# Kernel optimization log

Hardware: AMD Instinct MI355X
Metric: run time of the kernel (lower is better)

The kernel has to match this reference:

```python
import jax, jax.numpy as jnp
import numpy as np

B, T, DIM = 4, 2048, 1024
H, DH = 16, 64  # num_heads, dim_head; weight_dim = H*DH = 1024
SCALE = DIM ** (-0.5)  # note: original scales by dim**-0.5, not dim_head**-0.5


def setup_inputs() -> dict:
    key = jax.random.key(0)
    k1, k2, k3 = jax.random.split(key, 3)
    x = jax.random.normal(k1, (B, T, DIM), dtype=jnp.float32)
    w_qkv = jax.random.normal(k2, (3 * H * DH, DIM), dtype=jnp.float32) * (DIM ** -0.5)
    w_out = jax.random.normal(k3, (DIM, H * DH), dtype=jnp.float32) * ((H * DH) ** -0.5)
    b_out = jnp.zeros((DIM,), dtype=jnp.float32)
    return {"x": x, "w_qkv": w_qkv, "w_out": w_out, "b_out": b_out}


def reference(x, w_qkv, w_out, b_out):
    # qkv: [b, t, 3*H*DH] (torch Linear: x @ W^T)
    qkv = jnp.einsum('btc,oc->bto', x, w_qkv)
    # rearrange 'b t (d k h) -> k b h t d' with k=3, h=H: d is the OUTERMOST
    # factor of the flattened axis, then k, then h (h fastest-varying).
    qkv = qkv.reshape(B, T, DH, 3, H)          # [b, t, d, k, h]
    qkv = jnp.transpose(qkv, (3, 0, 4, 1, 2))   # [k, b, h, t, d]
    q, k, v = qkv[0], qkv[1], qkv[2]
    # scores: [b, h, t, t]
    attn = jnp.einsum('bhid,bhjd->bhij', q, k) * SCALE
    attn = jax.nn.softmax(attn, axis=-1)
    out = jnp.einsum('bhij,bhjd->bhid', attn, v)           # [b, h, t, d]
    out = jnp.transpose(out, (0, 2, 1, 3)).reshape(B, T, H * DH)  # 'b h t d -> b t (h d)'
    return jnp.einsum('btc,oc->bto', out, w_out) + b_out
```

## Files before the change

### kernel.cpp

```cpp
#include <hip/hip_runtime.h>
#include <hip/hip_bf16.h>


typedef __attribute__((ext_vector_type(8))) short short8;
typedef __attribute__((ext_vector_type(4))) float floatx4;
typedef __attribute__((ext_vector_type(16))) float floatx16;

static __device__ __forceinline__ floatx4 mfma16(short8 a, short8 b, floatx4 c) {
    return __builtin_amdgcn_mfma_f32_16x16x32_bf16(a, b, c, 0, 0, 0);
}
static __device__ __forceinline__ floatx16 mfma32(short8 a, short8 b, floatx16 c) {
    return __builtin_amdgcn_mfma_f32_32x32x16_bf16(a, b, c, 0, 0, 0);
}

static __device__ __forceinline__ unsigned short f2bf_bits(float f) {
    __hip_bfloat16 h = __float2bfloat16(f);
    return *reinterpret_cast<unsigned short*>(&h);
}

static __device__ __forceinline__ float fast_exp2(float x) {
#if __has_builtin(__builtin_amdgcn_exp2f)
    return __builtin_amdgcn_exp2f(x);
#else
    return exp2f(x);
#endif
}

static __device__ __forceinline__ unsigned cvt_pk_bf16(float lo, float hi) {
    unsigned r;
    asm("v_cvt_pk_bf16_f32 %0, %1, %2" : "=v"(r) : "v"(lo), "v"(hi));
    return r;
}

static __device__ __forceinline__ void plane32_swap(unsigned& x, unsigned& y) {
#if __has_builtin(__builtin_amdgcn_permlane32_swap)
    typedef unsigned int uintx2 __attribute__((ext_vector_type(2)));
    uintx2 r = __builtin_amdgcn_permlane32_swap(x, y, false, false);
    x = r[0];
    y = r[1];
#else
    asm volatile("v_permlane32_swap_b32 %0, %1" : "+v"(x), "+v"(y));
#endif
}

#define GLD16(gptr, ldsptr)                                                  \
    __builtin_amdgcn_global_load_lds(                                        \
        (const __attribute__((address_space(1))) void*)(gptr),               \
        (__attribute__((address_space(3))) void*)(ldsptr), 16, 0, 0)

__global__ __launch_bounds__(256) void k_cvt(
    const float* __restrict__ src, unsigned short* __restrict__ dst, int n4)
{
    typedef __attribute__((ext_vector_type(4))) unsigned short ushort4v;
    for (int i = blockIdx.x * blockDim.x + threadIdx.x; i < n4;
         i += gridDim.x * blockDim.x) {
        const float4 v = ((const float4*)src)[i];
        ushort4v o;
        o.x = f2bf_bits(v.x);
        o.y = f2bf_bits(v.y);
        o.z = f2bf_bits(v.z);
        o.w = f2bf_bits(v.w);
        ((ushort4v*)dst)[i] = o;
    }
}

__global__ __launch_bounds__(256) void k_qkv(
    const unsigned short* __restrict__ x,
    const unsigned short* __restrict__ wq,
    unsigned short* __restrict__ qb,
    unsigned short* __restrict__ kb,
    unsigned short* __restrict__ vb)
{
    __shared__ unsigned short SM[16384];

    const int tid  = threadIdx.x;
    const int wave = tid >> 6, lane = tid & 63;
    const int quad = lane >> 4, l16 = lane & 15;
    const int wm = wave >> 1, wn = wave & 1;

    const int fid  = blockIdx.y * 24 + blockIdx.x;
    const int nfid = (fid & 7) * 192 + (fid >> 3);
    const int bx = nfid % 24;
    const int m0 = (nfid / 24) * 128;
    const int kk = bx >> 3;
    const int cb = bx & 7;

    const int srow = lane >> 2;
    const int sc8  = (lane & 3) * 8;
    const int row0 = wave * 32 + srow;
    const int row1 = row0 + 16;
    int bn0, bn1;
    if (kk < 2) {
        bn0 = (row0 & 63) * 48 + kk * 16 + cb * 2 + (row0 >> 6);
        bn1 = (row1 & 63) * 48 + kk * 16 + cb * 2 + (row1 >> 6);
    } else {
        bn0 = (cb * 8 + (row0 >> 4)) * 48 + 32 + (row0 & 15);
        bn1 = (cb * 8 + (row1 >> 4)) * 48 + 32 + (row1 & 15);
    }

    floatx4 acc[4][4];
#pragma unroll
    for (int i = 0; i < 4; i++)
#pragma unroll
        for (int j = 0; j < 4; j++) acc[i][j] = (floatx4){0.f, 0.f, 0.f, 0.f};

#define QKV_STAGE(BUF, K0)                                                        \
    do {                                                                          \
        GLD16(&x[(m0 + row0) * 1024 + (K0) + sc8],                                \
              &SM[(BUF) * 8192 + (wave * 32) * 32]);                              \
        GLD16(&x[(m0 + row1) * 1024 + (K0) + sc8],                                \
              &SM[(BUF) * 8192 + (wave * 32 + 16) * 32]);                         \
        GLD16(&wq[bn0 * 1024 + (K0) + sc8],                                       \
              &SM[(BUF) * 8192 + 4096 + (wave * 32) * 32]);                       \
        GLD16(&wq[bn1 * 1024 + (K0) + sc8],                                       \
              &SM[(BUF) * 8192 + 4096 + (wave * 32 + 16) * 32]);                  \
    } while (0)

    QKV_STAGE(0, 0);
    int buf = 0;
    for (int k0 = 0; k0 < 1024; k0 += 32) {
        __syncthreads();
        if (k0 + 32 < 1024) QKV_STAGE(buf ^ 1, k0 + 32);

        const unsigned short* Ab = &SM[buf * 8192];
        const unsigned short* Bb = &SM[buf * 8192 + 4096];
        short8 af[4], bfv[4];
#pragma unroll
        for (int mi = 0; mi < 4; mi++)
            af[mi] = *(const short8*)&Ab[(wm * 64 + mi * 16 + l16) * 32 + quad * 8];
#pragma unroll
        for (int ni = 0; ni < 4; ni++)
            bfv[ni] = *(const short8*)&Bb[(wn * 64 + ni * 16 + l16) * 32 + quad * 8];
#pragma unroll
        for (int mi = 0; mi < 4; mi++)
#pragma unroll
            for (int ni = 0; ni < 4; ni++)
                acc[mi][ni] = mfma16(af[mi], bfv[ni], acc[mi][ni]);
        buf ^= 1;
    }
    __syncthreads();

    if (kk == 2) {
#pragma unroll
        for (int ni = 0; ni < 4; ni++) {
            const int d = cb * 8 + wn * 4 + ni;
#pragma unroll
            for (int mi = 0; mi < 4; mi++) {
                const int m  = m0 + wm * 64 + mi * 16 + quad * 4;
                const int b  = m >> 11;
                const int tt = m & 2047;
                ushort4 pk;
                pk.x = f2bf_bits(acc[mi][ni][0]);
                pk.y = f2bf_bits(acc[mi][ni][1]);
                pk.z = f2bf_bits(acc[mi][ni][2]);
                pk.w = f2bf_bits(acc[mi][ni][3]);
                *(ushort4*)&vb[((b * 16 + l16) * 64 + d) * 2048 + tt] = pk;
            }
        }
    } else {
        const float scale = (kk == 0) ? 0.045084220027780106f : 1.0f;
        unsigned short* dst = (kk == 0) ? qb : kb;
        const int b = m0 >> 11, tt0 = m0 & 2047;
#pragma unroll
        for (int s = 0; s < 2; s++) {
            if (wn == s) {
#pragma unroll
                for (int ni = 0; ni < 4; ni++) {
                    const int d = ni * 16 + l16;
#pragma unroll
                    for (int mi = 0; mi < 4; mi++) {
                        const int tl = wm * 64 + mi * 16 + quad * 4;
#pragma unroll
                        for (int r = 0; r < 4; r++)
                            SM[(tl + r) * 72 + d] = f2bf_bits(acc[mi][ni][r] * scale);
                    }
                }
            }
            __syncthreads();
#pragma unroll
            for (int u = 0; u < 4; u++) {
                const int w  = tid + u * 256;
                const int tl = w >> 3;
                const int ch = (w & 7) * 8;
                *(uint4*)&dst[((b * 16 + cb * 2 + s) * 2048 + tt0 + tl) * 64 + ch] =
                    *(const uint4*)&SM[tl * 72 + ch];
            }
            __syncthreads();
        }
    }
#undef QKV_STAGE
}

__global__ __launch_bounds__(256, 2) void k_attn(
    const unsigned short* __restrict__ qt,
    const unsigned short* __restrict__ kt,
    const unsigned short* __restrict__ vg,
    __hip_bfloat16* __restrict__ og)
{
    __shared__ unsigned short Ks[64 * 72];
    __shared__ unsigned short Vt[64 * 72];

    const int tid  = threadIdx.x;
    const int wave = tid >> 6, lane = tid & 63;
    const int l31  = lane & 31, hi = lane >> 5;
    const int blk = blockIdx.x;
    const int bh  = (blk & 7) | ((blk >> 6) << 3);
    const int q0  = ((blk >> 3) & 7) * 256;
    const int qr  = q0 + wave * 64;

    short8 qf[2][4];
#pragma unroll
    for (int qb2 = 0; qb2 < 2; qb2++)
#pragma unroll
        for (int ks = 0; ks < 4; ks++)
            qf[qb2][ks] = *(const short8*)
                &qt[(bh * 2048 + qr + qb2 * 32 + l31) * 64 + ks * 16 + hi * 8];

    float lsum[2] = {0.f, 0.f};
    floatx16 o[2][2];
#pragma unroll
    for (int qb2 = 0; qb2 < 2; qb2++)
#pragma unroll
        for (int db = 0; db < 2; db++)
#pragma unroll
            for (int r = 0; r < 16; r++) o[qb2][db][r] = 0.f;

    const int sr = tid >> 2, sc = (tid & 3) * 16;

    uint4 rka = *(const uint4*)&kt[(bh * 2048 + sr) * 64 + sc];
    uint4 rkb = *(const uint4*)&kt[(bh * 2048 + sr) * 64 + sc + 8];
    uint4 rva = *(const uint4*)&vg[(bh * 64 + sr) * 2048 + sc];
    uint4 rvb = *(const uint4*)&vg[(bh * 64 + sr) * 2048 + sc + 8];

    for (int j0 = 0; j0 < 2048; j0 += 64) {
        *(uint4*)&Ks[sr * 72 + sc]     = rka;
        *(uint4*)&Ks[sr * 72 + sc + 8] = rkb;
        *(uint4*)&Vt[sr * 72 + sc]     = rva;
        *(uint4*)&Vt[sr * 72 + sc + 8] = rvb;
        __syncthreads();
        if (j0 + 64 < 2048) {
            rka = *(const uint4*)&kt[(bh * 2048 + j0 + 64 + sr) * 64 + sc];
            rkb = *(const uint4*)&kt[(bh * 2048 + j0 + 64 + sr) * 64 + sc + 8];
            rva = *(const uint4*)&vg[(bh * 64 + sr) * 2048 + j0 + 64 + sc];
            rvb = *(const uint4*)&vg[(bh * 64 + sr) * 2048 + j0 + 64 + sc + 8];
        }

#pragma unroll
        for (int kb2 = 0; kb2 < 2; kb2++) {
            short8 kf[4];
#pragma unroll
            for (int ks = 0; ks < 4; ks++)
                kf[ks] = *(const short8*)
                    &Ks[(kb2 * 32 + l31) * 72 + ks * 16 + hi * 8];

            floatx16 st[2];
#pragma unroll
            for (int qb2 = 0; qb2 < 2; qb2++)
#pragma unroll
                for (int r = 0; r < 16; r++) st[qb2][r] = 0.f;
            __builtin_amdgcn_s_setprio(1);
#pragma unroll
            for (int ks = 0; ks < 4; ks++)
#pragma unroll
                for (int qb2 = 0; qb2 < 2; qb2++)
                    st[qb2] = mfma32(kf[ks], qf[qb2][ks], st[qb2]);
            __builtin_amdgcn_s_setprio(0);

            short8 paf[2][2];
#pragma unroll
            for (int qb2 = 0; qb2 < 2; qb2++) {
                float p[16];
#pragma unroll
                for (int r = 0; r < 16; r++) p[r] = fast_exp2(st[qb2][r]);
                lsum[qb2] += ((p[0] + p[1]) + (p[2] + p[3])) +
                             ((p[4] + p[5]) + (p[6] + p[7])) +
                             ((p[8] + p[9]) + (p[10] + p[11])) +
                             ((p[12] + p[13]) + (p[14] + p[15]));
#pragma unroll
                for (int hf = 0; hf < 2; hf++) {
                    const int r0 = hf * 8;
                    unsigned c01 = cvt_pk_bf16(p[r0 + 0], p[r0 + 1]);
                    unsigned c23 = cvt_pk_bf16(p[r0 + 2], p[r0 + 3]);
                    unsigned c45 = cvt_pk_bf16(p[r0 + 4], p[r0 + 5]);
                    unsigned c67 = cvt_pk_bf16(p[r0 + 6], p[r0 + 7]);
                    plane32_swap(c01, c45);
                    plane32_swap(c23, c67);
                    uint4 t4 = {c01, c23, c45, c67};
                    paf[qb2][hf] = *reinterpret_cast<short8*>(&t4);
                }
            }

            short8 vf[2][2];
#pragma unroll
            for (int db = 0; db < 2; db++)
#pragma unroll
                for (int hf = 0; hf < 2; hf++)
                    vf[db][hf] = *(const short8*)
                        &Vt[(db * 32 + l31) * 72 + kb2 * 32 + hf * 16 + hi * 8];
            __builtin_amdgcn_s_setprio(1);
#pragma unroll
            for (int qb2 = 0; qb2 < 2; qb2++)
#pragma unroll
                for (int db = 0; db < 2; db++)
#pragma unroll
                    for (int hf = 0; hf < 2; hf++)
                        o[qb2][db] = mfma32(paf[qb2][hf], vf[db][hf], o[qb2][db]);
            __builtin_amdgcn_s_setprio(0);
        }
        __syncthreads();
    }

    lsum[0] += __shfl_xor(lsum[0], 32);
    lsum[1] += __shfl_xor(lsum[1], 32);

    const int b = bh >> 4, h = bh & 15;
#pragma unroll
    for (int qb2 = 0; qb2 < 2; qb2++) {
#pragma unroll
        for (int r = 0; r < 16; r++) {
            const int qrl = (r & 3) + 8 * (r >> 2) + 4 * hi;
            const float inv = 1.0f / __shfl(lsum[qb2], qrl);
            const int t = qr + qb2 * 32 + qrl;
#pragma unroll
            for (int db = 0; db < 2; db++)
                og[(b * 2048 + t) * 1024 + h * 64 + db * 32 + l31] =
                    __float2bfloat16(o[qb2][db][r] * inv);
        }
    }
}

__global__ __launch_bounds__(256) void k_out(
    const unsigned short* __restrict__ a,
    const unsigned short* __restrict__ wq,
    const float* __restrict__ bias,
    float* __restrict__ out)
{
    __shared__ unsigned short SM[16384];

    const int tid  = threadIdx.x;
    const int wave = tid >> 6, lane = tid & 63;
    const int quad = lane >> 4, l16 = lane & 15;
    const int wm = wave >> 1, wn = wave & 1;

    const int fid  = blockIdx.y * 8 + blockIdx.x;
    const int nfid = (fid & 7) * 64 + (fid >> 3);
    const int n0 = (nfid & 7) * 128;
    const int m0 = (nfid >> 3) * 128;

    const int srow = lane >> 2;
    const int sc8  = (lane & 3) * 8;
    const int row0 = wave * 32 + srow;
    const int row1 = row0 + 16;

    floatx4 acc[4][4];
#pragma unroll
    for (int i = 0; i < 4; i++)
#pragma unroll
        for (int j = 0; j < 4; j++) acc[i][j] = (floatx4){0.f, 0.f, 0.f, 0.f};

#define OUT_STAGE(BUF, K0)                                                        \
    do {                                                                          \
        GLD16(&a[(m0 + row0) * 1024 + (K0) + sc8],                                \
              &SM[(BUF) * 8192 + (wave * 32) * 32]);                              \
        GLD16(&a[(m0 + row1) * 1024 + (K0) + sc8],                                \
              &SM[(BUF) * 8192 + (wave * 32 + 16) * 32]);                         \
        GLD16(&wq[(n0 + row0) * 1024 + (K0) + sc8],                               \
              &SM[(BUF) * 8192 + 4096 + (wave * 32) * 32]);                       \
        GLD16(&wq[(n0 + row1) * 1024 + (K0) + sc8],                               \
              &SM[(BUF) * 8192 + 4096 + (wave * 32 + 16) * 32]);                  \
    } while (0)

    OUT_STAGE(0, 0);
    int buf = 0;
    for (int k0 = 0; k0 < 1024; k0 += 32) {
        __syncthreads();
        if (k0 + 32 < 1024) OUT_STAGE(buf ^ 1, k0 + 32);

        const unsigned short* Ab = &SM[buf * 8192];
        const unsigned short* Bb = &SM[buf * 8192 + 4096];
        short8 af[4], bfv[4];
#pragma unroll
        for (int mi = 0; mi < 4; mi++)
            af[mi] = *(const short8*)&Ab[(wm * 64 + mi * 16 + l16) * 32 + quad * 8];
#pragma unroll
        for (int ni = 0; ni < 4; ni++)
            bfv[ni] = *(const short8*)&Bb[(wn * 64 + ni * 16 + l16) * 32 + quad * 8];
#pragma unroll
        for (int mi = 0; mi < 4; mi++)
#pragma unroll
            for (int ni = 0; ni < 4; ni++)
                acc[mi][ni] = mfma16(af[mi], bfv[ni], acc[mi][ni]);
        buf ^= 1;
    }
#undef OUT_STAGE

#pragma unroll
    for (int ni = 0; ni < 4; ni++) {
        const int col = n0 + wn * 64 + ni * 16 + l16;
        const float bv = bias[col];
#pragma unroll
        for (int mi = 0; mi < 4; mi++) {
            const int mbase = m0 + wm * 64 + mi * 16 + quad * 4;
#pragma unroll
            for (int r = 0; r < 4; r++)
                out[(mbase + r) * 1024 + col] = acc[mi][ni][r] + bv;
        }
    }
}

extern "C" void kernel_launch(void* const* d_in, const int* in_sizes, int n_in,
                              void* d_out, int out_size, void* d_ws, size_t ws_size,
                              hipStream_t stream) {
    const float* x    = (const float*)d_in[0];
    const float* wqkv = (const float*)d_in[1];
    const float* wout = (const float*)d_in[2];
    const float* bout = (const float*)d_in[3];
    float* out = (float*)d_out;

    unsigned short* ws = (unsigned short*)d_ws;
    unsigned short* xb    = ws;
    unsigned short* wqkvb = xb + 8388608;
    unsigned short* woutb = wqkvb + 3145728;
    unsigned short* qb    = woutb + 1048576;
    unsigned short* kb    = qb + 8388608;
    unsigned short* vb    = kb + 8388608;
    unsigned short* ob    = vb + 8388608;

    k_cvt<<<2048, 256, 0, stream>>>(x,    xb,    8388608 / 4);
    k_cvt<<<1024, 256, 0, stream>>>(wqkv, wqkvb, 3145728 / 4);
    k_cvt<<<512,  256, 0, stream>>>(wout, woutb, 1048576 / 4);

    k_qkv<<<dim3(24, 64), 256, 0, stream>>>(xb, wqkvb, qb, kb, vb);
    k_attn<<<512, 256, 0, stream>>>(qb, kb, vb, (__hip_bfloat16*)ob);
    k_out<<<dim3(8, 64), 256, 0, stream>>>(ob, woutb, bout, out);
}
```

Measured before the change: 254.2 us.

## Halve attention query tile per wave to double grid and occupancy

Each wave in the attention kernel now handles 32 query rows instead of 64, so each block covers 128 queries. The grid doubles to 1024 blocks and launch bounds ask for 4 blocks per CU. This cuts register pressure and is meant to hide latency through more resident waves. In exchange, every K/V tile is loaded and staged in LDS twice as often per query, and each wave does fewer MFMAs per LDS read.

After: 281.8 us. 1.11x slower.

```diff
diff --git a/kernel.cpp b/kernel.cpp
--- a/kernel.cpp
+++ b/kernel.cpp
@@ -191,7 +191,7 @@
 #undef QKV_STAGE
 }
 
-__global__ __launch_bounds__(256, 2) void k_attn(
+__global__ __launch_bounds__(256, 4) void k_attn(
     const unsigned short* __restrict__ qt,
     const unsigned short* __restrict__ kt,
     const unsigned short* __restrict__ vg,
@@ -204,26 +204,22 @@
     const int wave = tid >> 6, lane = tid & 63;
     const int l31  = lane & 31, hi = lane >> 5;
     const int blk = blockIdx.x;
-    const int bh  = (blk & 7) | ((blk >> 6) << 3);
-    const int q0  = ((blk >> 3) & 7) * 256;
-    const int qr  = q0 + wave * 64;
-
-    short8 qf[2][4];
-#pragma unroll
-    for (int qb2 = 0; qb2 < 2; qb2++)
-#pragma unroll
-        for (int ks = 0; ks < 4; ks++)
-            qf[qb2][ks] = *(const short8*)
-                &qt[(bh * 2048 + qr + qb2 * 32 + l31) * 64 + ks * 16 + hi * 8];
-
-    float lsum[2] = {0.f, 0.f};
-    floatx16 o[2][2];
-#pragma unroll
-    for (int qb2 = 0; qb2 < 2; qb2++)
-#pragma unroll
-        for (int db = 0; db < 2; db++)
-#pragma unroll
-            for (int r = 0; r < 16; r++) o[qb2][db][r] = 0.f;
+    const int bh  = (blk & 7) | ((blk >> 7) << 3);
+    const int q0  = ((blk >> 3) & 15) * 128;
+    const int qr  = q0 + wave * 32;
+
+    short8 qf[4];
+#pragma unroll
+    for (int ks = 0; ks < 4; ks++)
+        qf[ks] = *(const short8*)
+            &qt[(bh * 2048 + qr + l31) * 64 + ks * 16 + hi * 8];
+
+    float lsum = 0.f;
+    floatx16 o[2];
+#pragma unroll
+    for (int db = 0; db < 2; db++)
+#pragma unroll
+        for (int r = 0; r < 16; r++) o[db][r] = 0.f;
 
     const int sr = tid >> 2, sc = (tid & 3) * 16;
 
@@ -253,41 +249,34 @@
                 kf[ks] = *(const short8*)
                     &Ks[(kb2 * 32 + l31) * 72 + ks * 16 + hi * 8];
 
-            floatx16 st[2];
-#pragma unroll
-            for (int qb2 = 0; qb2 < 2; qb2++)
-#pragma unroll
-                for (int r = 0; r < 16; r++) st[qb2][r] = 0.f;
+            floatx16 st;
+#pragma unroll
+            for (int r = 0; r < 16; r++) st[r] = 0.f;
             __builtin_amdgcn_s_setprio(1);
 #pragma unroll
             for (int ks = 0; ks < 4; ks++)
-#pragma unroll
-                for (int qb2 = 0; qb2 < 2; qb2++)
-                    st[qb2] = mfma32(kf[ks], qf[qb2][ks], st[qb2]);
+                st = mfma32(kf[ks], qf[ks], st);
             __builtin_amdgcn_s_setprio(0);
 
-            short8 paf[2][2];
-#pragma unroll
-            for (int qb2 = 0; qb2 < 2; qb2++) {
-                float p[16];
-#pragma unroll
-                for (int r = 0; r < 16; r++) p[r] = fast_exp2(st[qb2][r]);
-                lsum[qb2] += ((p[0] + p[1]) + (p[2] + p[3])) +
-                             ((p[4] + p[5]) + (p[6] + p[7])) +
-                             ((p[8] + p[9]) + (p[10] + p[11])) +
-                             ((p[12] + p[13]) + (p[14] + p[15]));
-#pragma unroll
-                for (int hf = 0; hf < 2; hf++) {
-                    const int r0 = hf * 8;
-                    unsigned c01 = cvt_pk_bf16(p[r0 + 0], p[r0 + 1]);
-                    unsigned c23 = cvt_pk_bf16(p[r0 + 2], p[r0 + 3]);
-                    unsigned c45 = cvt_pk_bf16(p[r0 + 4], p[r0 + 5]);
-                    unsigned c67 = cvt_pk_bf16(p[r0 + 6], p[r0 + 7]);
-                    plane32_swap(c01, c45);
-                    plane32_swap(c23, c67);
-                    uint4 t4 = {c01, c23, c45, c67};
-                    paf[qb2][hf] = *reinterpret_cast<short8*>(&t4);
-                }
+            float p[16];
+#pragma unroll
+            for (int r = 0; r < 16; r++) p[r] = fast_exp2(st[r]);
+            lsum += (((p[0] + p[1]) + (p[2] + p[3])) +
+                     ((p[4] + p[5]) + (p[6] + p[7]))) +
+                    (((p[8] + p[9]) + (p[10] + p[11])) +
+                     ((p[12] + p[13]) + (p[14] + p[15])));
+            short8 paf[2];
+#pragma unroll
+            for (int hf = 0; hf < 2; hf++) {
+                const int r0 = hf * 8;
+                unsigned c01 = cvt_pk_bf16(p[r0 + 0], p[r0 + 1]);
+                unsigned c23 = cvt_pk_bf16(p[r0 + 2], p[r0 + 3]);
+                unsigned c45 = cvt_pk_bf16(p[r0 + 4], p[r0 + 5]);
+                unsigned c67 = cvt_pk_bf16(p[r0 + 6], p[r0 + 7]);
+                plane32_swap(c01, c45);
+                plane32_swap(c23, c67);
+                uint4 t4 = {c01, c23, c45, c67};
+                paf[hf] = *reinterpret_cast<short8*>(&t4);
             }
 
             short8 vf[2][2];
@@ -299,33 +288,27 @@
                         &Vt[(db * 32 + l31) * 72 + kb2 * 32 + hf * 16 + hi * 8];
             __builtin_amdgcn_s_setprio(1);
 #pragma unroll
-            for (int qb2 = 0; qb2 < 2; qb2++)
-#pragma unroll
-                for (int db = 0; db < 2; db++)
-#pragma unroll
-                    for (int hf = 0; hf < 2; hf++)
-                        o[qb2][db] = mfma32(paf[qb2][hf], vf[db][hf], o[qb2][db]);
+            for (int db = 0; db < 2; db++)
+#pragma unroll
+                for (int hf = 0; hf < 2; hf++)
+                    o[db] = mfma32(paf[hf], vf[db][hf], o[db]);
             __builtin_amdgcn_s_setprio(0);
         }
         __syncthreads();
     }
 
-    lsum[0] += __shfl_xor(lsum[0], 32);
-    lsum[1] += __shfl_xor(lsum[1], 32);
+    lsum += __shfl_xor(lsum, 32);
 
     const int b = bh >> 4, h = bh & 15;
 #pragma unroll
-    for (int qb2 = 0; qb2 < 2; qb2++) {
-#pragma unroll
-        for (int r = 0; r < 16; r++) {
-            const int qrl = (r & 3) + 8 * (r >> 2) + 4 * hi;
-            const float inv = 1.0f / __shfl(lsum[qb2], qrl);
-            const int t = qr + qb2 * 32 + qrl;
-#pragma unroll
-            for (int db = 0; db < 2; db++)
-                og[(b * 2048 + t) * 1024 + h * 64 + db * 32 + l31] =
-                    __float2bfloat16(o[qb2][db][r] * inv);
-        }
+    for (int r = 0; r < 16; r++) {
+        const int qrl = (r & 3) + 8 * (r >> 2) + 4 * hi;
+        const float inv = 1.0f / __shfl(lsum, qrl);
+        const int t = qr + qrl;
+#pragma unroll
+        for (int db = 0; db < 2; db++)
+            og[(b * 2048 + t) * 1024 + h * 64 + db * 32 + l31] =
+                __float2bfloat16(o[db][r] * inv);
     }
 }
 
@@ -431,6 +414,6 @@
     k_cvt<<<512,  256, 0, stream>>>(wout, woutb, 1048576 / 4);
 
     k_qkv<<<dim3(24, 64), 256, 0, stream>>>(xb, wqkvb, qb, kb, vb);
-    k_attn<<<512, 256, 0, stream>>>(qb, kb, vb, (__hip_bfloat16*)ob);
+    k_attn<<<1024, 256, 0, stream>>>(qb, kb, vb, (__hip_bfloat16*)ob);
     k_out<<<dim3(8, 64), 256, 0, stream>>>(ob, woutb, bout, out);
 }
```

## Load K/V fragments directly from global memory, dropping LDS staging and barriers

Applied to the files above, without the earlier changes.

The attention kernel stops staging K and V tiles through shared memory with register prefetch and block barriers. Each wave now reads its MFMA K and V fragments straight from global memory, relying on L2/L1 caching, and processes 32 keys per iteration with an unroll of 2. This removes LDS traffic and __syncthreads, but each of the four waves now fetches the same K/V data separately. It also loses the explicit prefetch overlap, so global load latency may be exposed.

Result: slower. 312.1 us (+22.8%).

```diff
diff --git a/kernel.cpp b/kernel.cpp
--- a/kernel.cpp
+++ b/kernel.cpp
@@ -197,9 +197,6 @@
     const unsigned short* __restrict__ vg,
     __hip_bfloat16* __restrict__ og)
 {
-    __shared__ unsigned short Ks[64 * 72];
-    __shared__ unsigned short Vt[64 * 72];
-
     const int tid  = threadIdx.x;
     const int wave = tid >> 6, lane = tid & 63;
     const int l31  = lane & 31, hi = lane >> 5;
@@ -225,89 +222,70 @@
 #pragma unroll
             for (int r = 0; r < 16; r++) o[qb2][db][r] = 0.f;
 
-    const int sr = tid >> 2, sc = (tid & 3) * 16;
-
-    uint4 rka = *(const uint4*)&kt[(bh * 2048 + sr) * 64 + sc];
-    uint4 rkb = *(const uint4*)&kt[(bh * 2048 + sr) * 64 + sc + 8];
-    uint4 rva = *(const uint4*)&vg[(bh * 64 + sr) * 2048 + sc];
-    uint4 rvb = *(const uint4*)&vg[(bh * 64 + sr) * 2048 + sc + 8];
-
-    for (int j0 = 0; j0 < 2048; j0 += 64) {
-        *(uint4*)&Ks[sr * 72 + sc]     = rka;
-        *(uint4*)&Ks[sr * 72 + sc + 8] = rkb;
-        *(uint4*)&Vt[sr * 72 + sc]     = rva;
-        *(uint4*)&Vt[sr * 72 + sc + 8] = rvb;
-        __syncthreads();
-        if (j0 + 64 < 2048) {
-            rka = *(const uint4*)&kt[(bh * 2048 + j0 + 64 + sr) * 64 + sc];
-            rkb = *(const uint4*)&kt[(bh * 2048 + j0 + 64 + sr) * 64 + sc + 8];
-            rva = *(const uint4*)&vg[(bh * 64 + sr) * 2048 + j0 + 64 + sc];
-            rvb = *(const uint4*)&vg[(bh * 64 + sr) * 2048 + j0 + 64 + sc + 8];
+    const unsigned short* kbase = &kt[bh * 2048 * 64];
+    const unsigned short* vbase = &vg[bh * 64 * 2048];
+
+#pragma unroll 2
+    for (int j = 0; j < 2048; j += 32) {
+        short8 kf[4];
+#pragma unroll
+        for (int ks = 0; ks < 4; ks++)
+            kf[ks] = *(const short8*)&kbase[(j + l31) * 64 + ks * 16 + hi * 8];
+
+        floatx16 st[2];
+#pragma unroll
+        for (int qb2 = 0; qb2 < 2; qb2++)
+#pragma unroll
+            for (int r = 0; r < 16; r++) st[qb2][r] = 0.f;
+        __builtin_amdgcn_s_setprio(1);
+#pragma unroll
+        for (int ks = 0; ks < 4; ks++)
+#pragma unroll
+            for (int qb2 = 0; qb2 < 2; qb2++)
+                st[qb2] = mfma32(kf[ks], qf[qb2][ks], st[qb2]);
+        __builtin_amdgcn_s_setprio(0);
+
+        short8 vf[2][2];
+#pragma unroll
+        for (int db = 0; db < 2; db++)
+#pragma unroll
+            for (int hf = 0; hf < 2; hf++)
+                vf[db][hf] = *(const short8*)
+                    &vbase[(db * 32 + l31) * 2048 + j + hf * 16 + hi * 8];
+
+        short8 paf[2][2];
+#pragma unroll
+        for (int qb2 = 0; qb2 < 2; qb2++) {
+            float p[16];
+#pragma unroll
+            for (int r = 0; r < 16; r++) p[r] = fast_exp2(st[qb2][r]);
+            lsum[qb2] += (((p[0] + p[1]) + (p[2] + p[3])) +
+                          ((p[4] + p[5]) + (p[6] + p[7]))) +
+                         (((p[8] + p[9]) + (p[10] + p[11])) +
+                          ((p[12] + p[13]) + (p[14] + p[15])));
+#pragma unroll
+            for (int hf = 0; hf < 2; hf++) {
+                const int r0 = hf * 8;
+                unsigned c01 = cvt_pk_bf16(p[r0 + 0], p[r0 + 1]);
+                unsigned c23 = cvt_pk_bf16(p[r0 + 2], p[r0 + 3]);
+                unsigned c45 = cvt_pk_bf16(p[r0 + 4], p[r0 + 5]);
+                unsigned c67 = cvt_pk_bf16(p[r0 + 6], p[r0 + 7]);
+                plane32_swap(c01, c45);
+                plane32_swap(c23, c67);
+                uint4 t4 = {c01, c23, c45, c67};
+                paf[qb2][hf] = *reinterpret_cast<short8*>(&t4);
+            }
         }
 
-#pragma unroll
-        for (int kb2 = 0; kb2 < 2; kb2++) {
-            short8 kf[4];
-#pragma unroll
-            for (int ks = 0; ks < 4; ks++)
-                kf[ks] = *(const short8*)
-                    &Ks[(kb2 * 32 + l31) * 72 + ks * 16 + hi * 8];
-
-            floatx16 st[2];
-#pragma unroll
-            for (int qb2 = 0; qb2 < 2; qb2++)
-#pragma unroll
-                for (int r = 0; r < 16; r++) st[qb2][r] = 0.f;
-            __builtin_amdgcn_s_setprio(1);
-#pragma unroll
-            for (int ks = 0; ks < 4; ks++)
-#pragma unroll
-                for (int qb2 = 0; qb2 < 2; qb2++)
-                    st[qb2] = mfma32(kf[ks], qf[qb2][ks], st[qb2]);
-            __builtin_amdgcn_s_setprio(0);
-
-            short8 paf[2][2];
-#pragma unroll
-            for (int qb2 = 0; qb2 < 2; qb2++) {
-                float p[16];
-#pragma unroll
-                for (int r = 0; r < 16; r++) p[r] = fast_exp2(st[qb2][r]);
-                lsum[qb2] += ((p[0] + p[1]) + (p[2] + p[3])) +
-                             ((p[4] + p[5]) + (p[6] + p[7])) +
-                             ((p[8] + p[9]) + (p[10] + p[11])) +
-                             ((p[12] + p[13]) + (p[14] + p[15]));
-#pragma unroll
-                for (int hf = 0; hf < 2; hf++) {
-                    const int r0 = hf * 8;
-                    unsigned c01 = cvt_pk_bf16(p[r0 + 0], p[r0 + 1]);
-                    unsigned c23 = cvt_pk_bf16(p[r0 + 2], p[r0 + 3]);
-                    unsigned c45 = cvt_pk_bf16(p[r0 + 4], p[r0 + 5]);
-                    unsigned c67 = cvt_pk_bf16(p[r0 + 6], p[r0 + 7]);
-                    plane32_swap(c01, c45);
-                    plane32_swap(c23, c67);
-                    uint4 t4 = {c01, c23, c45, c67};
-                    paf[qb2][hf] = *reinterpret_cast<short8*>(&t4);
-                }
-            }
-
-            short8 vf[2][2];
+        __builtin_amdgcn_s_setprio(1);
+#pragma unroll
+        for (int qb2 = 0; qb2 < 2; qb2++)
 #pragma unroll
             for (int db = 0; db < 2; db++)
 #pragma unroll
                 for (int hf = 0; hf < 2; hf++)
-                    vf[db][hf] = *(const short8*)
-                        &Vt[(db * 32 + l31) * 72 + kb2 * 32 + hf * 16 + hi * 8];
-            __builtin_amdgcn_s_setprio(1);
-#pragma unroll
-            for (int qb2 = 0; qb2 < 2; qb2++)
-#pragma unroll
-                for (int db = 0; db < 2; db++)
-#pragma unroll
-                    for (int hf = 0; hf < 2; hf++)
-                        o[qb2][db] = mfma32(paf[qb2][hf], vf[db][hf], o[qb2][db]);
-            __builtin_amdgcn_s_setprio(0);
-        }
-        __syncthreads();
+                    o[qb2][db] = mfma32(paf[qb2][hf], vf[db][hf], o[qb2][db]);
+        __builtin_amdgcn_s_setprio(0);
     }
 
     lsum[0] += __shfl_xor(lsum[0], 32);
```

## Triple-buffer GEMM LDS staging with partial vmcnt waits; lighter attention barriers

Applied to the files above, without the earlier changes.

The QKV and output-projection GEMMs move from a double-buffered LDS pipeline to a three-stage ring. Each iteration waits only for the oldest outstanding global-to-LDS loads (vmcnt(4)) before the barrier, so two tiles stay in flight while the current one is computed. The attention kernel swaps __syncthreads for raw s_barrier with explicit waitcnt and sched_barrier, cutting the implicit full waits. The cost is 50% more LDS per GEMM block, which may lower occupancy, and correctness now depends on the hand-placed waitcnt values.

Measured after the change: 268.4 us. +5.6%, slower.

```diff
diff --git a/kernel.cpp b/kernel.cpp
--- a/kernel.cpp
+++ b/kernel.cpp
@@ -71,7 +71,7 @@
     unsigned short* __restrict__ kb,
     unsigned short* __restrict__ vb)
 {
-    __shared__ unsigned short SM[16384];
+    __shared__ unsigned short SM[24576];
 
     const int tid  = threadIdx.x;
     const int wave = tid >> 6, lane = tid & 63;
@@ -117,13 +117,19 @@
     } while (0)
 
     QKV_STAGE(0, 0);
-    int buf = 0;
-    for (int k0 = 0; k0 < 1024; k0 += 32) {
-        __syncthreads();
-        if (k0 + 32 < 1024) QKV_STAGE(buf ^ 1, k0 + 32);
-
-        const unsigned short* Ab = &SM[buf * 8192];
-        const unsigned short* Bb = &SM[buf * 8192 + 4096];
+    QKV_STAGE(1, 32);
+    for (int i = 0; i < 32; ++i) {
+        if (i < 31) {
+            asm volatile("s_waitcnt vmcnt(4)" ::: "memory");
+        } else {
+            asm volatile("s_waitcnt vmcnt(0)" ::: "memory");
+        }
+        __builtin_amdgcn_s_barrier();
+        __builtin_amdgcn_sched_barrier(0);
+        if (i < 30) QKV_STAGE((i + 2) % 3, (i + 2) * 32);
+
+        const unsigned short* Ab = &SM[(i % 3) * 8192];
+        const unsigned short* Bb = Ab + 4096;
         short8 af[4], bfv[4];
 #pragma unroll
         for (int mi = 0; mi < 4; mi++)
@@ -136,7 +142,6 @@
 #pragma unroll
             for (int ni = 0; ni < 4; ni++)
                 acc[mi][ni] = mfma16(af[mi], bfv[ni], acc[mi][ni]);
-        buf ^= 1;
     }
     __syncthreads();
 
@@ -237,7 +242,9 @@
         *(uint4*)&Ks[sr * 72 + sc + 8] = rkb;
         *(uint4*)&Vt[sr * 72 + sc]     = rva;
         *(uint4*)&Vt[sr * 72 + sc + 8] = rvb;
-        __syncthreads();
+        asm volatile("s_waitcnt lgkmcnt(0)" ::: "memory");
+        __builtin_amdgcn_s_barrier();
+        __builtin_amdgcn_sched_barrier(0);
         if (j0 + 64 < 2048) {
             rka = *(const uint4*)&kt[(bh * 2048 + j0 + 64 + sr) * 64 + sc];
             rkb = *(const uint4*)&kt[(bh * 2048 + j0 + 64 + sr) * 64 + sc + 8];
@@ -272,10 +279,10 @@
                 float p[16];
 #pragma unroll
                 for (int r = 0; r < 16; r++) p[r] = fast_exp2(st[qb2][r]);
-                lsum[qb2] += ((p[0] + p[1]) + (p[2] + p[3])) +
-                             ((p[4] + p[5]) + (p[6] + p[7])) +
-                             ((p[8] + p[9]) + (p[10] + p[11])) +
-                             ((p[12] + p[13]) + (p[14] + p[15]));
+                lsum[qb2] += (((p[0] + p[1]) + (p[2] + p[3])) +
+                              ((p[4] + p[5]) + (p[6] + p[7]))) +
+                             (((p[8] + p[9]) + (p[10] + p[11])) +
+                              ((p[12] + p[13]) + (p[14] + p[15])));
 #pragma unroll
                 for (int hf = 0; hf < 2; hf++) {
                     const int r0 = hf * 8;
@@ -307,7 +314,9 @@
                         o[qb2][db] = mfma32(paf[qb2][hf], vf[db][hf], o[qb2][db]);
             __builtin_amdgcn_s_setprio(0);
         }
-        __syncthreads();
+        asm volatile("" ::: "memory");
+        __builtin_amdgcn_s_barrier();
+        __builtin_amdgcn_sched_barrier(0);
     }
 
     lsum[0] += __shfl_xor(lsum[0], 32);
@@ -335,7 +344,7 @@
     const float* __restrict__ bias,
     float* __restrict__ out)
 {
-    __shared__ unsigned short SM[16384];
+    __shared__ unsigned short SM[24576];
 
     const int tid  = threadIdx.x;
     const int wave = tid >> 6, lane = tid & 63;
@@ -371,13 +380,19 @@
     } while (0)
 
     OUT_STAGE(0, 0);
-    int buf = 0;
-    for (int k0 = 0; k0 < 1024; k0 += 32) {
-        __syncthreads();
-        if (k0 + 32 < 1024) OUT_STAGE(buf ^ 1, k0 + 32);
-
-        const unsigned short* Ab = &SM[buf * 8192];
-        const unsigned short* Bb = &SM[buf * 8192 + 4096];
+    OUT_STAGE(1, 32);
+    for (int i = 0; i < 32; ++i) {
+        if (i < 31) {
+            asm volatile("s_waitcnt vmcnt(4)" ::: "memory");
+        } else {
+            asm volatile("s_waitcnt vmcnt(0)" ::: "memory");
+        }
+        __builtin_amdgcn_s_barrier();
+        __builtin_amdgcn_sched_barrier(0);
+        if (i < 30) OUT_STAGE((i + 2) % 3, (i + 2) * 32);
+
+        const unsigned short* Ab = &SM[(i % 3) * 8192];
+        const unsigned short* Bb = Ab + 4096;
         short8 af[4], bfv[4];
 #pragma unroll
         for (int mi = 0; mi < 4; mi++)
@@ -390,7 +405,6 @@
 #pragma unroll
             for (int ni = 0; ni < 4; ni++)
                 acc[mi][ni] = mfma16(af[mi], bfv[ni], acc[mi][ni]);
-        buf ^= 1;
     }
 #undef OUT_STAGE
 
```
